# Optimization experiments

Hardware: AMD Instinct MI355X
Metric: run time of the kernel (lower is better)

Reference implementation:

```python
import jax, jax.numpy as jnp
import numpy as np

WS = 7          # window size
DIM = 192
HEADS = 6
NW = 64         # number of windows per image (mask leading dim)
NC = 3          # n_contrast (q and kv)
B_ = 1024       # num_windows * batch


def _relative_position_index(ws):
    coords = np.stack(np.meshgrid(np.arange(ws), np.arange(ws), indexing='ij'))  # (2, ws, ws)
    cf = coords.reshape(2, -1)                       # (2, ws*ws)
    rel = cf[:, :, None] - cf[:, None, :]            # (2, N, N)
    rel = rel.transpose(1, 2, 0).copy()              # (N, N, 2)
    rel[:, :, 0] += ws - 1
    rel[:, :, 1] += ws - 1
    rel[:, :, 0] *= 2 * ws - 1
    return rel.sum(-1)                               # (N, N) int

REL_IDX = jnp.asarray(_relative_position_index(WS))


def setup_inputs() -> dict:
    key = jax.random.key(0)
    ks = jax.random.split(key, 13)
    f32 = jnp.float32
    inp = {
        'x_q': jax.random.normal(ks[0], (B_, NC, WS, WS, DIM), f32),
        'x_k': jax.random.normal(ks[1], (B_, NC, WS, WS, DIM), f32),
        'x_v': jax.random.normal(ks[2], (B_, NC, WS, WS, DIM), f32),
        'mask': jax.random.normal(ks[3], (NW, WS * WS, WS * WS), f32),
        # Linear weights stored torch-style: (out_features, in_features)
        'q_w': jax.random.normal(ks[4], (DIM, DIM), f32) * 0.02,
        'q_b': jnp.zeros((DIM,), f32),
        'k_w': jax.random.normal(ks[5], (DIM, DIM), f32) * 0.02,
        'k_b': jnp.zeros((DIM,), f32),
        'v_w': jax.random.normal(ks[6], (DIM, DIM), f32) * 0.02,
        'v_b': jnp.zeros((DIM,), f32),
        'proj_w': jax.random.normal(ks[7], (DIM, DIM), f32) * 0.02,
        'proj_b': jnp.zeros((DIM,), f32),
        'bias_table': jax.random.normal(ks[8], ((2 * WS - 1) ** 2, HEADS), f32) * 0.02,
    }
    return inp


def reference(x_q, x_k, x_v, mask, q_w, q_b, k_w, k_b, v_w, v_b, proj_w, proj_b, bias_table):
    Bw, ncq, Wh, Ww, C = x_q.shape
    nckv = x_k.shape[1]
    H = HEADS
    hd = C // H
    Nq = ncq * Wh * Ww
    Nkv = nckv * Wh * Ww

    xq = x_q.reshape(Bw, Nq, C)
    xk = x_k.reshape(Bw, Nkv, C)
    xv = x_v.reshape(Bw, Nkv, C)

    q = (xq @ q_w.T + q_b).reshape(Bw, Nq, H, hd).transpose(0, 2, 1, 3)   # (B_, H, Nq, hd)
    k = (xk @ k_w.T + k_b).reshape(Bw, Nkv, H, hd).transpose(0, 2, 1, 3)
    v = (xv @ v_w.T + v_b).reshape(Bw, Nkv, H, hd).transpose(0, 2, 1, 3)

    scale = hd ** (-0.5)
    attn = jnp.einsum('bhqd,bhkd->bhqk', q * scale, k)                    # (B_, H, Nq, Nkv)

    Nwin = Wh * Ww
    bias = bias_table[REL_IDX.reshape(-1)].reshape(Nwin, Nwin, H)
    bias = bias.transpose(2, 0, 1)                                        # (H, Nwin, Nwin)
    bias = jnp.tile(bias, (1, ncq, nckv))                                 # (H, Nq, Nkv)
    attn = attn + bias[None]

    nW = mask.shape[0]
    m = jnp.tile(mask, (1, ncq, nckv))                                    # (nW, Nq, Nkv)
    attn = attn.reshape(Bw // nW, nW, H, Nq, Nkv) + m[None, :, None]
    attn = attn.reshape(Bw, H, Nq, Nkv)
    attn = jax.nn.softmax(attn, axis=-1)

    out = jnp.einsum('bhqk,bhkd->bhqd', attn, v)                          # (B_, H, Nq, hd)
    out = out.transpose(0, 2, 1, 3).reshape(Bw, Nq, C)
    out = out @ proj_w.T + proj_b
    return out.reshape(Bw, ncq, Wh, Ww, C)
```

## Files before the change

### kernel.cpp

```cpp
#include <hip/hip_runtime.h>
#include <stdint.h>

#define ROWS 150528
#define QSCALE 0.17677669529663687f
#define L2E 1.44269504088896f

typedef __attribute__((ext_vector_type(8))) __bf16 bf16x8;
typedef __attribute__((ext_vector_type(4))) __bf16 bf16x4;
typedef __attribute__((ext_vector_type(4))) float f32x4;
typedef __attribute__((ext_vector_type(4))) float f4;

static __device__ __forceinline__ f32x4 mfma_bf16(bf16x8 a, bf16x8 b, f32x4 c) {
  return __builtin_amdgcn_mfma_f32_16x16x32_bf16(a, b, c, 0, 0, 0);
}

static __device__ __forceinline__ uint32_t pack_bf16(float a, float b) {
  uint16_t ux = __builtin_bit_cast(uint16_t, (__bf16)a);
  uint16_t uy = __builtin_bit_cast(uint16_t, (__bf16)b);
  return (uint32_t)ux | ((uint32_t)uy << 16);
}

__global__ void cvt4(const float* s0, const float* s1, const float* s2, const float* s3,
                     __bf16* d0, __bf16* d1, __bf16* d2, __bf16* d3) {
  const int y = blockIdx.y;
  const float* s = y == 0 ? s0 : y == 1 ? s1 : y == 2 ? s2 : s3;
  __bf16* d = y == 0 ? d0 : y == 1 ? d1 : y == 2 ? d2 : d3;
  int i = blockIdx.x * 256 + threadIdx.x;
  f4 v = ((const f4*)s)[i];
  bf16x4 b;
  b[0] = (__bf16)v[0]; b[1] = (__bf16)v[1]; b[2] = (__bf16)v[2]; b[3] = (__bf16)v[3];
  ((bf16x4*)d)[i] = b;
}

__global__ void bmpre(const float* __restrict__ maskp, const float* __restrict__ btab,
                      float* __restrict__ bmall) {
  const int win = blockIdx.x, h = blockIdx.y;
  float* dst = bmall + ((size_t)(win * 6 + h)) * 2800;
  for (int i = threadIdx.x; i < 2796; i += 256) {
    int q = i / 57, ke = i - q * 57;
    int k = ke >= 49 ? ke - 49 : ke;
    if (q > 48) q = 48;
    int qi = q / 7, qj = q - qi * 7, ki = k / 7, kj = k - ki * 7;
    int rel = (qi - ki + 6) * 13 + (qj - kj + 6);
    dst[i] = (maskp[win * 2401 + q * 49 + k] + btab[rel * 6 + h]) * L2E;
  }
}

template<bool IN_F32, bool OUT_F32>
static __device__ __forceinline__
void gemm_body(const void* __restrict__ Xv, const __bf16* __restrict__ Wb,
               const float* __restrict__ bias, void* __restrict__ Ov, float scale,
               __bf16* Xs )
{
  const int tid = threadIdx.x;
  const int wv = tid >> 6, lane = tid & 63, lr = lane & 15, lg = lane >> 4;
  const size_t row0 = (size_t)blockIdx.x * 64;

  if (IN_F32) {
    const f4* X4 = (const f4*)Xv + row0 * 48;
    #pragma unroll
    for (int p = 0; p < 12; ++p) {
      int i = tid + p * 256;
      int r = i / 48, c = i % 48;
      f4 v = X4[i];
      bf16x4 bb;
      bb[0] = (__bf16)v[0]; bb[1] = (__bf16)v[1]; bb[2] = (__bf16)v[2]; bb[3] = (__bf16)v[3];
      *(bf16x4*)&Xs[r * 200 + c * 4] = bb;
    }
  } else {
    const __bf16* X = (const __bf16*)Xv;
    #pragma unroll
    for (int p = 0; p < 6; ++p) {
      int i = tid + p * 256;
      int r = i / 24, c8 = i % 24;
      int hh = c8 >> 2, sub = c8 & 3;
      *(bf16x8*)&Xs[r * 200 + c8 * 8] =
          *(const bf16x8*)&X[((size_t)hh * ROWS + row0 + r) * 32 + sub * 8];
    }
  }
  __syncthreads();

  #pragma unroll
  for (int t = 0; t < 3; ++t) {
    const int nt = wv + 4 * t;
    bf16x8 wf[6];
    const __bf16* wr = &Wb[(nt * 16 + lr) * 192 + lg * 8];
    #pragma unroll
    for (int kk = 0; kk < 6; ++kk) wf[kk] = *(const bf16x8*)&wr[kk * 32];
    const float bcol = bias[nt * 16 + lr] * scale;

    #pragma unroll
    for (int rg = 0; rg < 4; ++rg) {
      bf16x8 a[6];
      const __bf16* xr = &Xs[(rg * 16 + lr) * 200 + lg * 8];
      #pragma unroll
      for (int kk = 0; kk < 6; ++kk) a[kk] = *(const bf16x8*)&xr[kk * 32];
      f32x4 acc = {0.f, 0.f, 0.f, 0.f};
      #pragma unroll
      for (int kk = 0; kk < 6; ++kk) acc = mfma_bf16(a[kk], wf[kk], acc);
      const size_t grow = row0 + rg * 16 + lg * 4;
      if (OUT_F32) {
        const int col = nt * 16 + lr;
        #pragma unroll
        for (int j = 0; j < 4; ++j)
          ((float*)Ov)[(grow + j) * 192 + col] = acc[j] * scale + bcol;
      } else {
        const int hh = nt >> 1, c32 = (nt & 1) * 16 + lr;
        #pragma unroll
        for (int j = 0; j < 4; ++j)
          ((__bf16*)Ov)[((size_t)hh * ROWS + grow + j) * 32 + c32] =
              (__bf16)(acc[j] * scale + bcol);
      }
    }
  }
}

__global__ __launch_bounds__(256, 3)
void qkvgemm(const float* __restrict__ xq, const float* __restrict__ xk,
             const float* __restrict__ xv,
             const __bf16* __restrict__ wq, const __bf16* __restrict__ wk,
             const __bf16* __restrict__ wv,
             const float* __restrict__ bq, const float* __restrict__ bk,
             const float* __restrict__ bv,
             __bf16* __restrict__ oq, __bf16* __restrict__ ok,
             __bf16* __restrict__ ov)
{
  __shared__ __align__(16) __bf16 Xs[64 * 200];
  const int y = blockIdx.y;
  const float* x = y == 0 ? xq : y == 1 ? xk : xv;
  const __bf16* w = y == 0 ? wq : y == 1 ? wk : wv;
  const float* bi = y == 0 ? bq : y == 1 ? bk : bv;
  __bf16* o = y == 0 ? oq : y == 1 ? ok : ov;
  const float scale = y == 0 ? (QSCALE * L2E) : 1.f;
  gemm_body<true, false>(x, w, bi, o, scale, Xs);
}

__global__ __launch_bounds__(256, 3)
void projgemm(const __bf16* __restrict__ X, const __bf16* __restrict__ Wb,
              const float* __restrict__ bias, float* __restrict__ Ov)
{
  __shared__ __align__(16) __bf16 Xs[64 * 200];
  gemm_body<false, true>(X, Wb, bias, Ov, 1.f, Xs);
}

__global__ __launch_bounds__(320, 5)
void attn8(const __bf16* __restrict__ Q, const __bf16* __restrict__ K,
           const __bf16* __restrict__ V, __bf16* __restrict__ O,
           const float* __restrict__ bmall)
{
  __shared__ __align__(16) __bf16 Ks[160 * 40];
  __shared__ __align__(16) __bf16 Vt[32 * 168];
  __shared__ __align__(16) float bm2[2796];

  const int b = blockIdx.x, h = blockIdx.y;
  const int tid = threadIdx.x;
  const size_t hb = (size_t)h * ROWS + (size_t)b * 147;
  const int wv = tid >> 6, lane = tid & 63;
  const int lr = lane & 15, lg = lane >> 4;

  bf16x8 qf = *(const bf16x8*)&Q[(hb + wv * 16 + lr) * 32 + lg * 8];

  {
    const f4* bsrc = (const f4*)(bmall + (size_t)((b & 63) * 6 + h) * 2800);
    for (int i = tid; i < 699; i += 320) ((f4*)bm2)[i] = bsrc[i];
  }
  for (int i = tid; i < 588; i += 320) {
    int k = i >> 2, c = i & 3;
    int phys = (k & ~31) | (((k >> 2) & 1) << 4) | (((k >> 3) & 3) << 2) | (k & 3);
    *(bf16x8*)&Ks[phys * 40 + c * 8] = *(const bf16x8*)&K[(hb + k) * 32 + c * 8];
  }
  for (int t = tid; t < 588; t += 320) {
    int key = t >> 2, dblk = t & 3;
    bf16x8 v = *(const bf16x8*)&V[(hb + key) * 32 + dblk * 8];
    #pragma unroll
    for (int e = 0; e < 8; ++e) Vt[(dblk * 8 + e) * 168 + key] = v[e];
  }
  for (int i = tid; i < 32 * 13; i += 320) {
    int d = i / 13, key = 147 + (i - (i / 13) * 13);
    Vt[d * 168 + key] = (__bf16)0.f;
  }
  __syncthreads();

  #pragma unroll
  for (int t = 0; t < 2; ++t) {
    const int mt = wv + 5 * t;

    bf16x8 qn = qf;
    if (t == 0) {
      int qr = (wv + 5) * 16 + lr; if (qr > 146) qr = 146;
      qn = *(const bf16x8*)&Q[(hb + qr) * 32 + lg * 8];
    }

    int r = mt * 16 + lr;
    int q49 = r; if (q49 >= 98) q49 -= 98; if (q49 >= 49) q49 -= 49;
    const float* bmrow = &bm2[q49 * 57];

    f32x4 o0 = {0.f,0.f,0.f,0.f}, o1 = {0.f,0.f,0.f,0.f};
    float sum = 0.f;
    int kb = lg * 8;
    #pragma unroll
    for (int s = 0; s < 5; ++s) {
      const f32x4 z = {0.f,0.f,0.f,0.f};
      f32x4 st0 = mfma_bf16(*(const bf16x8*)&Ks[(s * 32 + lr) * 40 + lg * 8], qf, z);
      f32x4 st1 = mfma_bf16(*(const bf16x8*)&Ks[(s * 32 + 16 + lr) * 40 + lg * 8], qf, z);
      const float* bp = bmrow + kb;
      #pragma unroll
      for (int j = 0; j < 4; ++j) { st0[j] += bp[j]; st1[j] += bp[4 + j]; }
      if (s == 4) {
        #pragma unroll
        for (int j = 0; j < 4; ++j) {
          if (lg * 8 + j >= 19) st0[j] = -1e30f;
          if (lg * 8 + j >= 15) st1[j] = -1e30f;
        }
      }
      #pragma unroll
      for (int j = 0; j < 4; ++j) { st0[j] = exp2f(st0[j]); sum += st0[j]; }
      #pragma unroll
      for (int j = 0; j < 4; ++j) { st1[j] = exp2f(st1[j]); sum += st1[j]; }
      union { bf16x8 v; uint32_t w[4]; } pu;
      pu.w[0] = pack_bf16(st0[0], st0[1]);
      pu.w[1] = pack_bf16(st0[2], st0[3]);
      pu.w[2] = pack_bf16(st1[0], st1[1]);
      pu.w[3] = pack_bf16(st1[2], st1[3]);
      bf16x8 v0 = *(const bf16x8*)&Vt[lr * 168 + s * 32 + lg * 8];
      bf16x8 v1 = *(const bf16x8*)&Vt[(16 + lr) * 168 + s * 32 + lg * 8];
      o0 = mfma_bf16(pu.v, v0, o0);
      o1 = mfma_bf16(pu.v, v1, o1);
      kb += 32; if (kb >= 49) kb -= 49;
    }
    sum += __shfl_xor(sum, 16);
    sum += __shfl_xor(sum, 32);
    const float rinv = 1.f / sum;
    #pragma unroll
    for (int j = 0; j < 4; ++j) {
      const int qa = mt * 16 + lg * 4 + j;
      const float rj = __shfl(rinv, lg * 4 + j);
      if (qa < 147) {
        const size_t base = (hb + qa) * 32;
        O[base + lr]      = (__bf16)(o0[j] * rj);
        O[base + 16 + lr] = (__bf16)(o1[j] * rj);
      }
    }
    qf = qn;
  }
}

extern "C" void kernel_launch(void* const* d_in, const int* in_sizes, int n_in,
                              void* d_out, int out_size, void* d_ws, size_t ws_size,
                              hipStream_t stream) {
  (void)in_sizes; (void)n_in; (void)out_size;
  const float* x_q  = (const float*)d_in[0];
  const float* x_k  = (const float*)d_in[1];
  const float* x_v  = (const float*)d_in[2];
  const float* maskp= (const float*)d_in[3];
  const float* q_w  = (const float*)d_in[4];
  const float* q_b  = (const float*)d_in[5];
  const float* k_w  = (const float*)d_in[6];
  const float* k_b  = (const float*)d_in[7];
  const float* v_w  = (const float*)d_in[8];
  const float* v_b  = (const float*)d_in[9];
  const float* p_w  = (const float*)d_in[10];
  const float* p_b  = (const float*)d_in[11];
  const float* btab = (const float*)d_in[12];

  char* ws = (char*)d_ws;
  float* bmall = (float*)ws;
  const size_t bmsz = (size_t)64 * 6 * 2800 * sizeof(float);
  char* wsp = ws + bmsz;
  const size_t wsz = 36864 * sizeof(__bf16);
  __bf16* wq  = (__bf16*)wsp;
  __bf16* wk  = (__bf16*)(wsp + wsz);
  __bf16* wvp = (__bf16*)(wsp + 2 * wsz);
  __bf16* wp  = (__bf16*)(wsp + 3 * wsz);
  char* bufs = wsp + 4 * wsz;
  const size_t sz = (size_t)ROWS * 192 * sizeof(__bf16);
  __bf16* qb = (__bf16*)bufs;
  __bf16* kb = (__bf16*)(bufs + sz);
  __bf16* vb = (__bf16*)(bufs + 2 * sz);
  const size_t need4 = bmsz + 4 * wsz + 4 * sz;
  __bf16* ob = (ws_size >= need4) ? (__bf16*)(bufs + 3 * sz) : qb;

  cvt4<<<dim3(36, 4), 256, 0, stream>>>(q_w, k_w, v_w, p_w, wq, wk, wvp, wp);
  bmpre<<<dim3(64, 6), 256, 0, stream>>>(maskp, btab, bmall);

  qkvgemm<<<dim3(ROWS / 64, 3), 256, 0, stream>>>(x_q, x_k, x_v, wq, wk, wvp,
                                                  q_b, k_b, v_b, qb, kb, vb);

  attn8<<<dim3(1024, 6), 320, 0, stream>>>(qb, kb, vb, ob, bmall);

  projgemm<<<ROWS / 64, 256, 0, stream>>>(ob, wp, p_b, (float*)d_out);
}
```

Measured before the change: 290.9 us.

## Process three row tiles per GEMM block with register-prefetched next tile

Each GEMM block now handles three consecutive 64-row tiles instead of one. The weight fragments and bias for all three column tiles are loaded into registers once per block. The next tile's input is prefetched into registers while the current tile's MFMAs run, then written to shared memory between barriers. This amortises weight loads and hides global-load latency, at the cost of higher register pressure (launch bounds drop from 3 to 2 blocks per CU) and a grid one third the size.

```diff
diff --git a/kernel.cpp b/kernel.cpp
--- a/kernel.cpp
+++ b/kernel.cpp
@@ -48,16 +48,28 @@
 
 template<bool IN_F32, bool OUT_F32>
 static __device__ __forceinline__
-void gemm_body(const void* __restrict__ Xv, const __bf16* __restrict__ Wb,
-               const float* __restrict__ bias, void* __restrict__ Ov, float scale,
-               __bf16* Xs )
+void gemm3t(const void* __restrict__ Xv, const __bf16* __restrict__ Wb,
+            const float* __restrict__ bias, void* __restrict__ Ov, float scale,
+            __bf16* Xs )
 {
   const int tid = threadIdx.x;
   const int wv = tid >> 6, lane = tid & 63, lr = lane & 15, lg = lane >> 4;
-  const size_t row0 = (size_t)blockIdx.x * 64;
+
+  bf16x8 wf[3][6];
+  float bcol[3];
+  #pragma unroll
+  for (int t = 0; t < 3; ++t) {
+    const int nt = wv + 4 * t;
+    const __bf16* wr = &Wb[(nt * 16 + lr) * 192 + lg * 8];
+    #pragma unroll
+    for (int kk = 0; kk < 6; ++kk) wf[t][kk] = *(const bf16x8*)&wr[kk * 32];
+    bcol[t] = bias[nt * 16 + lr] * scale;
+  }
+
+  const size_t ti0 = (size_t)blockIdx.x * 3;
 
   if (IN_F32) {
-    const f4* X4 = (const f4*)Xv + row0 * 48;
+    const f4* X4 = (const f4*)Xv + ti0 * 64 * 48;
     #pragma unroll
     for (int p = 0; p < 12; ++p) {
       int i = tid + p * 256;
@@ -75,19 +87,33 @@
       int r = i / 24, c8 = i % 24;
       int hh = c8 >> 2, sub = c8 & 3;
       *(bf16x8*)&Xs[r * 200 + c8 * 8] =
-          *(const bf16x8*)&X[((size_t)hh * ROWS + row0 + r) * 32 + sub * 8];
+          *(const bf16x8*)&X[((size_t)hh * ROWS + ti0 * 64 + r) * 32 + sub * 8];
     }
   }
   __syncthreads();
 
   #pragma unroll
-  for (int t = 0; t < 3; ++t) {
-    const int nt = wv + 4 * t;
-    bf16x8 wf[6];
-    const __bf16* wr = &Wb[(nt * 16 + lr) * 192 + lg * 8];
-    #pragma unroll
-    for (int kk = 0; kk < 6; ++kk) wf[kk] = *(const bf16x8*)&wr[kk * 32];
-    const float bcol = bias[nt * 16 + lr] * scale;
+  for (int it = 0; it < 3; ++it) {
+    const size_t row0 = (ti0 + it) * 64;
+
+    f4 pf[12];
+    bf16x8 pf8[6];
+    if (it < 2) {
+      if (IN_F32) {
+        const f4* X4n = (const f4*)Xv + (row0 + 64) * 48;
+        #pragma unroll
+        for (int p = 0; p < 12; ++p) pf[p] = X4n[tid + p * 256];
+      } else {
+        const __bf16* X = (const __bf16*)Xv;
+        #pragma unroll
+        for (int p = 0; p < 6; ++p) {
+          int i = tid + p * 256;
+          int r = i / 24, c8 = i % 24;
+          int hh = c8 >> 2, sub = c8 & 3;
+          pf8[p] = *(const bf16x8*)&X[((size_t)hh * ROWS + row0 + 64 + r) * 32 + sub * 8];
+        }
+      }
+    }
 
     #pragma unroll
     for (int rg = 0; rg < 4; ++rg) {
@@ -95,27 +121,54 @@
       const __bf16* xr = &Xs[(rg * 16 + lr) * 200 + lg * 8];
       #pragma unroll
       for (int kk = 0; kk < 6; ++kk) a[kk] = *(const bf16x8*)&xr[kk * 32];
-      f32x4 acc = {0.f, 0.f, 0.f, 0.f};
-      #pragma unroll
-      for (int kk = 0; kk < 6; ++kk) acc = mfma_bf16(a[kk], wf[kk], acc);
       const size_t grow = row0 + rg * 16 + lg * 4;
-      if (OUT_F32) {
-        const int col = nt * 16 + lr;
-        #pragma unroll
-        for (int j = 0; j < 4; ++j)
-          ((float*)Ov)[(grow + j) * 192 + col] = acc[j] * scale + bcol;
+      #pragma unroll
+      for (int t = 0; t < 3; ++t) {
+        f32x4 acc = {0.f, 0.f, 0.f, 0.f};
+        #pragma unroll
+        for (int kk = 0; kk < 6; ++kk) acc = mfma_bf16(a[kk], wf[t][kk], acc);
+        const int nt = wv + 4 * t;
+        if (OUT_F32) {
+          const int col = nt * 16 + lr;
+          #pragma unroll
+          for (int j = 0; j < 4; ++j)
+            ((float*)Ov)[(grow + j) * 192 + col] = acc[j] * scale + bcol[t];
+        } else {
+          const int hh = nt >> 1, c32 = (nt & 1) * 16 + lr;
+          #pragma unroll
+          for (int j = 0; j < 4; ++j)
+            ((__bf16*)Ov)[((size_t)hh * ROWS + grow + j) * 32 + c32] =
+                (__bf16)(acc[j] * scale + bcol[t]);
+        }
+      }
+    }
+
+    if (it < 2) {
+      __syncthreads();
+      if (IN_F32) {
+        #pragma unroll
+        for (int p = 0; p < 12; ++p) {
+          int i = tid + p * 256;
+          int r = i / 48, c = i % 48;
+          bf16x4 bb;
+          bb[0] = (__bf16)pf[p][0]; bb[1] = (__bf16)pf[p][1];
+          bb[2] = (__bf16)pf[p][2]; bb[3] = (__bf16)pf[p][3];
+          *(bf16x4*)&Xs[r * 200 + c * 4] = bb;
+        }
       } else {
-        const int hh = nt >> 1, c32 = (nt & 1) * 16 + lr;
-        #pragma unroll
-        for (int j = 0; j < 4; ++j)
-          ((__bf16*)Ov)[((size_t)hh * ROWS + grow + j) * 32 + c32] =
-              (__bf16)(acc[j] * scale + bcol);
-      }
-    }
-  }
-}
-
-__global__ __launch_bounds__(256, 3)
+        #pragma unroll
+        for (int p = 0; p < 6; ++p) {
+          int i = tid + p * 256;
+          int r = i / 24, c8 = i % 24;
+          *(bf16x8*)&Xs[r * 200 + c8 * 8] = pf8[p];
+        }
+      }
+      __syncthreads();
+    }
+  }
+}
+
+__global__ __launch_bounds__(256, 2)
 void qkvgemm(const float* __restrict__ xq, const float* __restrict__ xk,
              const float* __restrict__ xv,
              const __bf16* __restrict__ wq, const __bf16* __restrict__ wk,
@@ -132,15 +185,15 @@
   const float* bi = y == 0 ? bq : y == 1 ? bk : bv;
   __bf16* o = y == 0 ? oq : y == 1 ? ok : ov;
   const float scale = y == 0 ? (QSCALE * L2E) : 1.f;
-  gemm_body<true, false>(x, w, bi, o, scale, Xs);
-}
-
-__global__ __launch_bounds__(256, 3)
+  gemm3t<true, false>(x, w, bi, o, scale, Xs);
+}
+
+__global__ __launch_bounds__(256, 2)
 void projgemm(const __bf16* __restrict__ X, const __bf16* __restrict__ Wb,
               const float* __restrict__ bias, float* __restrict__ Ov)
 {
   __shared__ __align__(16) __bf16 Xs[64 * 200];
-  gemm_body<false, true>(X, Wb, bias, Ov, 1.f, Xs);
+  gemm3t<false, true>(X, Wb, bias, Ov, 1.f, Xs);
 }
 
 __global__ __launch_bounds__(320, 5)
@@ -283,10 +336,10 @@
   cvt4<<<dim3(36, 4), 256, 0, stream>>>(q_w, k_w, v_w, p_w, wq, wk, wvp, wp);
   bmpre<<<dim3(64, 6), 256, 0, stream>>>(maskp, btab, bmall);
 
-  qkvgemm<<<dim3(ROWS / 64, 3), 256, 0, stream>>>(x_q, x_k, x_v, wq, wk, wvp,
-                                                  q_b, k_b, v_b, qb, kb, vb);
+  qkvgemm<<<dim3(ROWS / 192, 3), 256, 0, stream>>>(x_q, x_k, x_v, wq, wk, wvp,
+                                                   q_b, k_b, v_b, qb, kb, vb);
 
   attn8<<<dim3(1024, 6), 320, 0, stream>>>(qb, kb, vb, ob, bmall);
 
-  projgemm<<<ROWS / 64, 256, 0, stream>>>(ob, wp, p_b, (float*)d_out);
-}
+  projgemm<<<ROWS / 192, 256, 0, stream>>>(ob, wp, p_b, (float*)d_out);
+}
```

Result: faster. 264.0 us (-9.3%).

## Load GEMM activations straight into registers, skipping LDS staging

Applied to the files above, without the earlier changes.

Rewrites the QKV and projection GEMMs so each wave loads its own 32 rows of activations directly from global memory into MFMA operand registers. This removes the shared-memory tile and its barrier. Each block now covers 128 rows, the grid is halved, and each wave loops over all 12 output column tiles. In exchange, every wave re-reads the full weight matrix, and the global loads of the fp32 input are strided per lane rather than coalesced across the block. Launch bounds drop to 2 blocks per SM to allow more registers.

```diff
diff --git a/kernel.cpp b/kernel.cpp
--- a/kernel.cpp
+++ b/kernel.cpp
@@ -48,57 +48,70 @@
 
 template<bool IN_F32, bool OUT_F32>
 static __device__ __forceinline__
-void gemm_body(const void* __restrict__ Xv, const __bf16* __restrict__ Wb,
-               const float* __restrict__ bias, void* __restrict__ Ov, float scale,
-               __bf16* Xs )
+void gemm_nolds(const void* __restrict__ Xv, const __bf16* __restrict__ Wb,
+                const float* __restrict__ bias, void* __restrict__ Ov, float scale)
 {
   const int tid = threadIdx.x;
   const int wv = tid >> 6, lane = tid & 63, lr = lane & 15, lg = lane >> 4;
-  const size_t row0 = (size_t)blockIdx.x * 64;
-
+  const size_t row0 = (size_t)blockIdx.x * 128 + wv * 32;
+
+  bf16x8 a[2][6];
   if (IN_F32) {
-    const f4* X4 = (const f4*)Xv + row0 * 48;
-    #pragma unroll
-    for (int p = 0; p < 12; ++p) {
-      int i = tid + p * 256;
-      int r = i / 48, c = i % 48;
-      f4 v = X4[i];
-      bf16x4 bb;
-      bb[0] = (__bf16)v[0]; bb[1] = (__bf16)v[1]; bb[2] = (__bf16)v[2]; bb[3] = (__bf16)v[3];
-      *(bf16x4*)&Xs[r * 200 + c * 4] = bb;
+    const float* X = (const float*)Xv;
+    {
+      f4 p[12];
+      #pragma unroll
+      for (int kk = 0; kk < 6; ++kk) {
+        const float* ba = &X[(row0 + lr) * 192 + kk * 32 + lg * 8];
+        p[2 * kk] = *(const f4*)ba;
+        p[2 * kk + 1] = *(const f4*)(ba + 4);
+      }
+      #pragma unroll
+      for (int kk = 0; kk < 6; ++kk)
+        #pragma unroll
+        for (int e = 0; e < 4; ++e) {
+          a[0][kk][e]     = (__bf16)p[2 * kk][e];
+          a[0][kk][4 + e] = (__bf16)p[2 * kk + 1][e];
+        }
+    }
+    {
+      f4 p[12];
+      #pragma unroll
+      for (int kk = 0; kk < 6; ++kk) {
+        const float* ba = &X[(row0 + 16 + lr) * 192 + kk * 32 + lg * 8];
+        p[2 * kk] = *(const f4*)ba;
+        p[2 * kk + 1] = *(const f4*)(ba + 4);
+      }
+      #pragma unroll
+      for (int kk = 0; kk < 6; ++kk)
+        #pragma unroll
+        for (int e = 0; e < 4; ++e) {
+          a[1][kk][e]     = (__bf16)p[2 * kk][e];
+          a[1][kk][4 + e] = (__bf16)p[2 * kk + 1][e];
+        }
     }
   } else {
     const __bf16* X = (const __bf16*)Xv;
     #pragma unroll
-    for (int p = 0; p < 6; ++p) {
-      int i = tid + p * 256;
-      int r = i / 24, c8 = i % 24;
-      int hh = c8 >> 2, sub = c8 & 3;
-      *(bf16x8*)&Xs[r * 200 + c8 * 8] =
-          *(const bf16x8*)&X[((size_t)hh * ROWS + row0 + r) * 32 + sub * 8];
-    }
-  }
-  __syncthreads();
-
-  #pragma unroll
-  for (int t = 0; t < 3; ++t) {
-    const int nt = wv + 4 * t;
+    for (int kk = 0; kk < 6; ++kk) {
+      a[0][kk] = *(const bf16x8*)&X[((size_t)kk * ROWS + row0 + lr) * 32 + lg * 8];
+      a[1][kk] = *(const bf16x8*)&X[((size_t)kk * ROWS + row0 + 16 + lr) * 32 + lg * 8];
+    }
+  }
+
+  #pragma unroll 1
+  for (int nt = 0; nt < 12; ++nt) {
     bf16x8 wf[6];
     const __bf16* wr = &Wb[(nt * 16 + lr) * 192 + lg * 8];
     #pragma unroll
     for (int kk = 0; kk < 6; ++kk) wf[kk] = *(const bf16x8*)&wr[kk * 32];
     const float bcol = bias[nt * 16 + lr] * scale;
-
-    #pragma unroll
-    for (int rg = 0; rg < 4; ++rg) {
-      bf16x8 a[6];
-      const __bf16* xr = &Xs[(rg * 16 + lr) * 200 + lg * 8];
-      #pragma unroll
-      for (int kk = 0; kk < 6; ++kk) a[kk] = *(const bf16x8*)&xr[kk * 32];
+    #pragma unroll
+    for (int g = 0; g < 2; ++g) {
       f32x4 acc = {0.f, 0.f, 0.f, 0.f};
       #pragma unroll
-      for (int kk = 0; kk < 6; ++kk) acc = mfma_bf16(a[kk], wf[kk], acc);
-      const size_t grow = row0 + rg * 16 + lg * 4;
+      for (int kk = 0; kk < 6; ++kk) acc = mfma_bf16(a[g][kk], wf[kk], acc);
+      const size_t grow = row0 + g * 16 + lg * 4;
       if (OUT_F32) {
         const int col = nt * 16 + lr;
         #pragma unroll
@@ -115,7 +128,7 @@
   }
 }
 
-__global__ __launch_bounds__(256, 3)
+__global__ __launch_bounds__(256, 2)
 void qkvgemm(const float* __restrict__ xq, const float* __restrict__ xk,
              const float* __restrict__ xv,
              const __bf16* __restrict__ wq, const __bf16* __restrict__ wk,
@@ -125,22 +138,20 @@
              __bf16* __restrict__ oq, __bf16* __restrict__ ok,
              __bf16* __restrict__ ov)
 {
-  __shared__ __align__(16) __bf16 Xs[64 * 200];
   const int y = blockIdx.y;
   const float* x = y == 0 ? xq : y == 1 ? xk : xv;
   const __bf16* w = y == 0 ? wq : y == 1 ? wk : wv;
   const float* bi = y == 0 ? bq : y == 1 ? bk : bv;
   __bf16* o = y == 0 ? oq : y == 1 ? ok : ov;
   const float scale = y == 0 ? (QSCALE * L2E) : 1.f;
-  gemm_body<true, false>(x, w, bi, o, scale, Xs);
-}
-
-__global__ __launch_bounds__(256, 3)
+  gemm_nolds<true, false>(x, w, bi, o, scale);
+}
+
+__global__ __launch_bounds__(256, 2)
 void projgemm(const __bf16* __restrict__ X, const __bf16* __restrict__ Wb,
               const float* __restrict__ bias, float* __restrict__ Ov)
 {
-  __shared__ __align__(16) __bf16 Xs[64 * 200];
-  gemm_body<false, true>(X, Wb, bias, Ov, 1.f, Xs);
+  gemm_nolds<false, true>(X, Wb, bias, Ov, 1.f);
 }
 
 __global__ __launch_bounds__(320, 5)
@@ -283,10 +294,10 @@
   cvt4<<<dim3(36, 4), 256, 0, stream>>>(q_w, k_w, v_w, p_w, wq, wk, wvp, wp);
   bmpre<<<dim3(64, 6), 256, 0, stream>>>(maskp, btab, bmall);
 
-  qkvgemm<<<dim3(ROWS / 64, 3), 256, 0, stream>>>(x_q, x_k, x_v, wq, wk, wvp,
-                                                  q_b, k_b, v_b, qb, kb, vb);
+  qkvgemm<<<dim3(ROWS / 128, 3), 256, 0, stream>>>(x_q, x_k, x_v, wq, wk, wvp,
+                                                   q_b, k_b, v_b, qb, kb, vb);
 
   attn8<<<dim3(1024, 6), 320, 0, stream>>>(qb, kb, vb, ob, bmall);
 
-  projgemm<<<ROWS / 64, 256, 0, stream>>>(ob, wp, p_b, (float*)d_out);
-}
+  projgemm<<<ROWS / 128, 256, 0, stream>>>(ob, wp, p_b, (float*)d_out);
+}
```

New measurement: 367.9 us. +26.5%, slower.
